# Performance work log

Hardware: AMD Instinct MI355X
Metric: run time of the kernel (lower is better)

Reference implementation:

```python
import jax, jax.numpy as jnp
import numpy as np

ALPHA = 0.2          # LeakyReLU negative slope
NEG_BIG = -9e15      # mask value from original code


def setup_inputs() -> dict:
    key = jax.random.key(0)
    k1, k2, k3, k4 = jax.random.split(key, 4)
    B, N, F_in, F_out = 16, 1024, 256, 256
    x = jax.random.normal(k1, (B, N, F_in), dtype=jnp.float32)
    adj = jax.random.randint(k2, (B, N, N), 0, 2, dtype=jnp.int32)
    # xavier-uniform-like scales
    W = jax.random.normal(k3, (F_in, F_out), dtype=jnp.float32) * np.sqrt(2.0 / (F_in + F_out))
    a = jax.random.normal(k4, (2 * F_out, 1), dtype=jnp.float32) * np.sqrt(2.0 / (2 * F_out + 1))
    return {"x": x, "adj": adj, "W": W, "a": a}


def reference(x, adj, W, a):
    # x: [B,N,Fin], adj: [B,N,N] (int mask), W: [Fin,Fout], a: [2*Fout,1]
    F_out = a.shape[0] // 2
    h = jnp.einsum("bni,io->bno", x, W)            # [B,N,Fout]
    # Decompose a into left/right halves: e_ij = lrelu(a_l.h_i + a_r.h_j)
    a_l = a[:F_out, 0]                               # [Fout]
    a_r = a[F_out:, 0]                               # [Fout]
    el = h @ a_l                                     # [B,N] score contribution of target i
    er = h @ a_r                                     # [B,N] score contribution of source j
    e = jax.nn.leaky_relu(el[:, :, None] + er[:, None, :], ALPHA)  # [B,N,N]
    e = jnp.where(adj > 0, e, NEG_BIG)
    attn = jax.nn.softmax(e, axis=-1)                # masked softmax over neighbors j
    # weighted sum of neighbor features; concat with n_heads=1 is identity
    return jnp.einsum("bij,bjo->bio", attn, h)       # [B,N,Fout]
```

## Files before the change

kernel.cpp:

```cpp
#include <hip/hip_runtime.h>
#include <stdint.h>

#define ALPHA 0.2f
#define NEG_BIG -9000000000000000.0f

typedef __attribute__((ext_vector_type(8))) short bf16x8;
typedef __attribute__((ext_vector_type(8))) unsigned short u16x8;
typedef __attribute__((ext_vector_type(4))) float f32x4;

__device__ __forceinline__ unsigned short f2bf(float f) {
    unsigned int u = __float_as_uint(f);
    u += 0x7fffu + ((u >> 16) & 1u);
    return (unsigned short)(u >> 16);
}

__device__ __forceinline__ void gload_lds16(const void* g, void* l) {
    __builtin_amdgcn_global_load_lds(
        (const __attribute__((address_space(1))) unsigned int*)g,
        (__attribute__((address_space(3))) unsigned int*)l, 16, 0, 0);
}

__global__ void wt_wa_kernel(const float* __restrict__ W,
                             const float* __restrict__ a,
                             unsigned short* __restrict__ Wtbf,
                             float* __restrict__ wa) {
    const int t = threadIdx.x;
    if (blockIdx.x < 256) {
        const int o = blockIdx.x;
        Wtbf[o * 256 + t] = f2bf(W[t * 256 + o]);
    } else {
        float sl = 0.f, sr = 0.f;
        const float* wr = W + t * 256;
        for (int o = 0; o < 256; ++o) {
            const float wv = wr[o];
            sl += wv * a[o];
            sr += wv * a[256 + o];
        }
        wa[t] = sl;
        wa[256 + t] = sr;
    }
}

__global__ __launch_bounds__(256) void eler2x_kernel(
    const float* __restrict__ x, const float* __restrict__ wa,
    float* __restrict__ el, float* __restrict__ er,
    unsigned short* __restrict__ xbf)
{
    const int w = threadIdx.x >> 6, l = threadIdx.x & 63;
    const int r = blockIdx.x * 4 + w;
    const float4 xv = *(const float4*)(x + (size_t)r * 256 + l * 4);
    const float4 al = *(const float4*)(wa + l * 4);
    const float4 ar = *(const float4*)(wa + 256 + l * 4);

    ushort4 xb;
    xb.x = f2bf(xv.x); xb.y = f2bf(xv.y); xb.z = f2bf(xv.z); xb.w = f2bf(xv.w);
    *(ushort4*)(xbf + (size_t)r * 256 + l * 4) = xb;

    float sl = xv.x * al.x + xv.y * al.y + xv.z * al.z + xv.w * al.w;
    float sr = xv.x * ar.x + xv.y * ar.y + xv.z * ar.z + xv.w * ar.w;
#pragma unroll
    for (int off = 32; off >= 1; off >>= 1) {
        sl += __shfl_xor(sl, off);
        sr += __shfl_xor(sr, off);
    }
    if (l == 0) { el[r] = sl; er[r] = sr; }
}

__global__ __launch_bounds__(256) void gemm_h(
    const unsigned short* __restrict__ A,
    const unsigned short* __restrict__ Bt,
    unsigned short* __restrict__ C)
{
    __shared__ __align__(16) unsigned short As[64 * 64];
    __shared__ __align__(16) unsigned short Bs[128 * 64];

    const int tid = threadIdx.x;
    const int w = tid >> 6, l = tid & 63;
    const int q = l >> 4, ml = l & 15;
    const int wm = (w >> 1) * 32;
    const int wn = (w & 1) * 64;
    const int m0 = blockIdx.y * 64;
    const int n0 = blockIdx.x * 128;

    f32x4 acc[2][4];
    for (int i = 0; i < 2; ++i)
        for (int j = 0; j < 4; ++j) {
            f32x4 z = {0.f, 0.f, 0.f, 0.f};
            acc[i][j] = z;
        }

    for (int k0 = 0; k0 < 256; k0 += 64) {
        for (int c = 0; c < 2; ++c) {
            const int cb = c * 256 + (w << 6);
            const int p = cb + l;
            const int r = p >> 3;
            const int cc = (p & 7) ^ (r & 7);
            gload_lds16(A + (size_t)(m0 + r) * 256 + k0 + cc * 8, As + cb * 8);
        }
        for (int c = 0; c < 4; ++c) {
            const int cb = c * 256 + (w << 6);
            const int p = cb + l;
            const int r = p >> 3;
            const int cc = (p & 7) ^ (r & 7);
            gload_lds16(Bt + (size_t)(n0 + r) * 256 + k0 + cc * 8, Bs + cb * 8);
        }
        __syncthreads();

        bf16x8 aF[2][2], bF[2][4];
#pragma unroll
        for (int ks = 0; ks < 2; ++ks) {
#pragma unroll
            for (int mt = 0; mt < 2; ++mt) {
                const int mm = wm + mt * 16 + ml;
                aF[ks][mt] = *(const bf16x8*)(As + (mm * 8 + ((ks * 4 + q) ^ (mm & 7))) * 8);
            }
#pragma unroll
            for (int nt = 0; nt < 4; ++nt) {
                const int nn = wn + nt * 16 + ml;
                bF[ks][nt] = *(const bf16x8*)(Bs + (nn * 8 + ((ks * 4 + q) ^ (nn & 7))) * 8);
            }
        }
#pragma unroll
        for (int ks = 0; ks < 2; ++ks)
            for (int mt = 0; mt < 2; ++mt)
                for (int nt = 0; nt < 4; ++nt)
                    acc[mt][nt] = __builtin_amdgcn_mfma_f32_16x16x32_bf16(
                        aF[ks][mt], bF[ks][nt], acc[mt][nt], 0, 0, 0);
        __syncthreads();
    }

    for (int mt = 0; mt < 2; ++mt)
        for (int nt = 0; nt < 4; ++nt) {
            const int gn = n0 + wn + nt * 16 + ml;
            for (int r = 0; r < 4; ++r) {
                const int gm = m0 + wm + mt * 16 + q * 4 + r;
                C[(size_t)gm * 16384 + gn] = f2bf(acc[mt][nt][r]);
            }
        }
}

__global__ __launch_bounds__(256) void mask_kernel(
    const int* __restrict__ adj,
    const float* __restrict__ el,
    const float* __restrict__ er,
    float* __restrict__ c,
    unsigned short* __restrict__ pk16)
{
    __shared__ unsigned char nibs[4][256];

    const int w = threadIdx.x >> 6, l = threadIdx.x & 63;
    const int row = blockIdx.x * 4 + w;
    const int b = row >> 10;
    const int* arow = adj + (size_t)row * 1024;
    const float* erb = er + (b << 10);
    const float eli = el[row];

    float ev[16];
    float m = -3.0e38f;
#pragma unroll
    for (int it = 0; it < 4; ++it) {
        const int j = it * 256 + l * 4;
        const int4 av = *(const int4*)(arow + j);
        const float4 erv = *(const float4*)(erb + j);
        float e0 = eli + erv.x; e0 = e0 > 0.f ? e0 : ALPHA * e0; e0 = av.x > 0 ? e0 : NEG_BIG;
        float e1 = eli + erv.y; e1 = e1 > 0.f ? e1 : ALPHA * e1; e1 = av.y > 0 ? e1 : NEG_BIG;
        float e2 = eli + erv.z; e2 = e2 > 0.f ? e2 : ALPHA * e2; e2 = av.z > 0 ? e2 : NEG_BIG;
        float e3 = eli + erv.w; e3 = e3 > 0.f ? e3 : ALPHA * e3; e3 = av.w > 0 ? e3 : NEG_BIG;
        ev[it * 4 + 0] = e0; ev[it * 4 + 1] = e1;
        ev[it * 4 + 2] = e2; ev[it * 4 + 3] = e3;
        m = fmaxf(m, fmaxf(fmaxf(e0, e1), fmaxf(e2, e3)));
        nibs[w][it * 64 + l] =
            (unsigned char)((av.x > 0) | ((av.y > 0) << 1) |
                            ((av.z > 0) << 2) | ((av.w > 0) << 3));
    }
#pragma unroll
    for (int off = 32; off >= 1; off >>= 1) m = fmaxf(m, __shfl_xor(m, off));
    float s = 0.f;
#pragma unroll
    for (int u = 0; u < 16; ++u) s += __expf(ev[u] - m);
#pragma unroll
    for (int off = 32; off >= 1; off >>= 1) s += __shfl_xor(s, off);
    if (l == 0) c[row] = m + __logf(s);

    const unsigned nr = *(const unsigned int*)(&nibs[w][l * 4]);
    const unsigned short mask16 =
        (unsigned short)((nr & 0xFu) | ((nr >> 4) & 0xF0u) |
                         ((nr >> 8) & 0xF00u) | ((nr >> 12) & 0xF000u));
    pk16[(size_t)row * 64 + l] = mask16;
}

__global__ __launch_bounds__(256) void pv_kernel(
    const unsigned short* __restrict__ pk16,
    const float* __restrict__ el,
    const float* __restrict__ er,
    const float* __restrict__ c,
    const unsigned short* __restrict__ hT,
    float* __restrict__ out)
{
    __shared__ float er_s[1024];
    __shared__ __align__(16) unsigned short pk_s[32 * 64];
    __shared__ __align__(16) unsigned short Hs[256 * 64];
    __shared__ __align__(16) unsigned short Ps[32 * 72];

    const int tid = threadIdx.x;
    const int w = tid >> 6, l = tid & 63;
    const int q = l >> 4, ml = l & 15;
    const int b = blockIdx.y;
    const int i0 = blockIdx.x * 32;

    *(float4*)(er_s + tid * 4) = *(const float4*)(er + (b << 10) + tid * 4);
    *(u16x8*)(pk_s + tid * 8) =
        *(const u16x8*)(pk16 + ((size_t)(b << 10) + i0) * 64 + tid * 8);
    const int ib = tid >> 3;
    const int js = (tid & 7) * 8;
    const float eli_b = el[(b << 10) + i0 + ib];
    const float ci = c[(b << 10) + i0 + ib];
    __syncthreads();

    f32x4 acc[2][4];
    for (int i = 0; i < 2; ++i)
        for (int j = 0; j < 4; ++j) {
            f32x4 z = {0.f, 0.f, 0.f, 0.f};
            acc[i][j] = z;
        }

    const unsigned short* hb = hT + (size_t)b * 1024;

    for (int j0 = 0; j0 < 1024; j0 += 64) {
        for (int cr = 0; cr < 8; ++cr) {
            const int cb = cr * 256 + (w << 6);
            const int p = cb + l;
            const int r = p >> 3;
            const int cc = (p & 7) ^ (r & 7);
            gload_lds16(hb + (size_t)r * 16384 + j0 + cc * 8, Hs + cb * 8);
        }
        {
            const unsigned hw = pk_s[ib * 64 + ((j0 + js) >> 4)];
            const unsigned v = (hw >> ((j0 + js) & 15)) & 0xFFu;
            u16x8 pvv;
#pragma unroll
            for (int u = 0; u < 8; ++u) {
                float e = eli_b + er_s[j0 + js + u];
                e = e > 0.f ? e : ALPHA * e;
                const float p = ((v >> u) & 1u) ? __expf(e - ci) : 0.f;
                pvv[u] = f2bf(p);
            }
            *(u16x8*)(Ps + ib * 72 + js) = pvv;
        }
        __syncthreads();

        bf16x8 aF[2][2], bF[2][4];
#pragma unroll
        for (int ks = 0; ks < 2; ++ks) {
#pragma unroll
            for (int mt = 0; mt < 2; ++mt)
                aF[ks][mt] = *(const bf16x8*)(Ps + (mt * 16 + ml) * 72 + ks * 32 + q * 8);
#pragma unroll
            for (int nt = 0; nt < 4; ++nt) {
                const int oc = (w << 6) + nt * 16 + ml;
                bF[ks][nt] = *(const bf16x8*)(Hs + (oc * 8 + ((ks * 4 + q) ^ (oc & 7))) * 8);
            }
        }
#pragma unroll
        for (int ks = 0; ks < 2; ++ks)
            for (int mt = 0; mt < 2; ++mt)
                for (int nt = 0; nt < 4; ++nt)
                    acc[mt][nt] = __builtin_amdgcn_mfma_f32_16x16x32_bf16(
                        aF[ks][mt], bF[ks][nt], acc[mt][nt], 0, 0, 0);
        __syncthreads();
    }

    float* ob = out + (size_t)b * 262144;
    for (int mt = 0; mt < 2; ++mt)
        for (int nt = 0; nt < 4; ++nt) {
            const int gn = (w << 6) + nt * 16 + ml;
            for (int r = 0; r < 4; ++r) {
                const int gm = i0 + mt * 16 + q * 4 + r;
                ob[(size_t)gm * 256 + gn] = acc[mt][nt][r];
            }
        }
}

extern "C" void kernel_launch(void* const* d_in, const int* in_sizes, int n_in,
                              void* d_out, int out_size, void* d_ws, size_t ws_size,
                              hipStream_t stream) {
    const float* x   = (const float*)d_in[0];
    const int*   adj = (const int*)d_in[1];
    const float* W   = (const float*)d_in[2];
    const float* a   = (const float*)d_in[3];
    float* out = (float*)d_out;

    char* ws = (char*)d_ws;
    unsigned short* Wtbf  = (unsigned short*)(ws);
    float* wa             = (float*)(ws + 131072);
    unsigned short* xbf   = (unsigned short*)(ws + 133120);
    unsigned short* h_T   = (unsigned short*)(ws + 8521728);
    float* el             = (float*)(ws + 16910336);
    float* er             = (float*)(ws + 16975872);
    float* c              = (float*)(ws + 17041408);
    unsigned short* pk16  = (unsigned short*)(ws + 17106944);

    wt_wa_kernel<<<dim3(257), dim3(256), 0, stream>>>(W, a, Wtbf, wa);

    eler2x_kernel<<<dim3(4096), dim3(256), 0, stream>>>(x, wa, el, er, xbf);

    gemm_h<<<dim3(128, 4), dim3(256), 0, stream>>>(Wtbf, xbf, h_T);

    mask_kernel<<<dim3(4096), dim3(256), 0, stream>>>(adj, el, er, c, pk16);

    pv_kernel<<<dim3(32, 16), dim3(256), 0, stream>>>(pk16, el, er, c, h_T, out);
}
```

Before: 156.3 us.

## Restructure PV kernel with direct-register H loads, double-buffered P tiles, exp2 scaling

The PV kernel now uses 512-thread blocks over 64 rows, with blocks mapped so batches are interleaved. It loads H fragments straight from global memory into registers, one tile ahead, instead of staging them through LDS. P tiles are double-buffered in LDS and guarded by a lighter barrier that waits only on LDS counters, so building the next P tile overlaps the MFMA work. Scores are prescaled by log2(e) so the kernels can call exp2/log2 directly, and the launch grid shrinks from 512 blocks to 256. The risks are uncoalesced H reads from global memory and reduced parallelism, since each block now covers more rows.

```diff
diff --git a/kernel.cpp b/kernel.cpp
--- a/kernel.cpp
+++ b/kernel.cpp
@@ -3,6 +3,7 @@
 
 #define ALPHA 0.2f
 #define NEG_BIG -9000000000000000.0f
+#define L2E 1.4426950408889634f
 
 typedef __attribute__((ext_vector_type(8))) short bf16x8;
 typedef __attribute__((ext_vector_type(8))) unsigned short u16x8;
@@ -18,6 +19,11 @@
     __builtin_amdgcn_global_load_lds(
         (const __attribute__((address_space(1))) unsigned int*)g,
         (__attribute__((address_space(3))) unsigned int*)l, 16, 0, 0);
+}
+
+__device__ __forceinline__ void bar_lds() {
+    asm volatile("s_waitcnt lgkmcnt(0)" ::: "memory");
+    __builtin_amdgcn_s_barrier();
 }
 
 __global__ void wt_wa_kernel(const float* __restrict__ W,
@@ -63,7 +69,7 @@
         sl += __shfl_xor(sl, off);
         sr += __shfl_xor(sr, off);
     }
-    if (l == 0) { el[r] = sl; er[r] = sr; }
+    if (l == 0) { el[r] = sl * L2E; er[r] = sr * L2E; }
 }
 
 __global__ __launch_bounds__(256) void gemm_h(
@@ -177,10 +183,10 @@
     for (int off = 32; off >= 1; off >>= 1) m = fmaxf(m, __shfl_xor(m, off));
     float s = 0.f;
 #pragma unroll
-    for (int u = 0; u < 16; ++u) s += __expf(ev[u] - m);
+    for (int u = 0; u < 16; ++u) s += exp2f(ev[u] - m);
 #pragma unroll
     for (int off = 32; off >= 1; off >>= 1) s += __shfl_xor(s, off);
-    if (l == 0) c[row] = m + __logf(s);
+    if (l == 0) c[row] = m + log2f(s);
 
     const unsigned nr = *(const unsigned int*)(&nibs[w][l * 4]);
     const unsigned short mask16 =
@@ -189,93 +195,129 @@
     pk16[(size_t)row * 64 + l] = mask16;
 }
 
-__global__ __launch_bounds__(256) void pv_kernel(
+__global__ __launch_bounds__(512, 2) void pv_kernel(
     const unsigned short* __restrict__ pk16,
-    const float* __restrict__ el,
-    const float* __restrict__ er,
-    const float* __restrict__ c,
+    const float* __restrict__ el2,
+    const float* __restrict__ er2,
+    const float* __restrict__ c2,
     const unsigned short* __restrict__ hT,
     float* __restrict__ out)
 {
     __shared__ float er_s[1024];
-    __shared__ __align__(16) unsigned short pk_s[32 * 64];
-    __shared__ __align__(16) unsigned short Hs[256 * 64];
-    __shared__ __align__(16) unsigned short Ps[32 * 72];
+    __shared__ __align__(16) unsigned short pk_s[64 * 72];
+    __shared__ __align__(16) unsigned short Ps[2 * 64 * 72];
 
     const int tid = threadIdx.x;
     const int w = tid >> 6, l = tid & 63;
     const int q = l >> 4, ml = l & 15;
-    const int b = blockIdx.y;
-    const int i0 = blockIdx.x * 32;
-
-    *(float4*)(er_s + tid * 4) = *(const float4*)(er + (b << 10) + tid * 4);
-    *(u16x8*)(pk_s + tid * 8) =
-        *(const u16x8*)(pk16 + ((size_t)(b << 10) + i0) * 64 + tid * 8);
+    const int wm = (w >> 2) * 32;
+    const int wn = (w & 3) * 64;
+
+    const int lin = blockIdx.x;
+    const int b = ((lin & 7) << 1) | ((lin >> 3) & 1);
+    const int i0 = (lin >> 4) * 64;
+
+    *(float2*)(er_s + tid * 2) = *(const float2*)(er2 + (b << 10) + tid * 2);
+    {
+        const int pr = tid >> 3, pc = (tid & 7) * 8;
+        *(u16x8*)(pk_s + pr * 72 + pc) =
+            *(const u16x8*)(pk16 + ((size_t)((b << 10) + i0 + pr)) * 64 + pc);
+    }
+
     const int ib = tid >> 3;
     const int js = (tid & 7) * 8;
-    const float eli_b = el[(b << 10) + i0 + ib];
-    const float ci = c[(b << 10) + i0 + ib];
-    __syncthreads();
+    const int rg = (b << 10) + i0 + ib;
+    const float el2i = el2[rg];
+    const float c2i = c2[rg];
 
     f32x4 acc[2][4];
+#pragma unroll
     for (int i = 0; i < 2; ++i)
+#pragma unroll
         for (int j = 0; j < 4; ++j) {
             f32x4 z = {0.f, 0.f, 0.f, 0.f};
             acc[i][j] = z;
         }
 
     const unsigned short* hb = hT + (size_t)b * 1024;
-
-    for (int j0 = 0; j0 < 1024; j0 += 64) {
-        for (int cr = 0; cr < 8; ++cr) {
-            const int cb = cr * 256 + (w << 6);
-            const int p = cb + l;
-            const int r = p >> 3;
-            const int cc = (p & 7) ^ (r & 7);
-            gload_lds16(hb + (size_t)r * 16384 + j0 + cc * 8, Hs + cb * 8);
-        }
-        {
-            const unsigned hw = pk_s[ib * 64 + ((j0 + js) >> 4)];
-            const unsigned v = (hw >> ((j0 + js) & 15)) & 0xFFu;
-            u16x8 pvv;
-#pragma unroll
-            for (int u = 0; u < 8; ++u) {
-                float e = eli_b + er_s[j0 + js + u];
-                e = e > 0.f ? e : ALPHA * e;
-                const float p = ((v >> u) & 1u) ? __expf(e - ci) : 0.f;
-                pvv[u] = f2bf(p);
-            }
-            *(u16x8*)(Ps + ib * 72 + js) = pvv;
-        }
-        __syncthreads();
-
-        bf16x8 aF[2][2], bF[2][4];
-#pragma unroll
-        for (int ks = 0; ks < 2; ++ks) {
-#pragma unroll
-            for (int mt = 0; mt < 2; ++mt)
-                aF[ks][mt] = *(const bf16x8*)(Ps + (mt * 16 + ml) * 72 + ks * 32 + q * 8);
-#pragma unroll
-            for (int nt = 0; nt < 4; ++nt) {
-                const int oc = (w << 6) + nt * 16 + ml;
-                bF[ks][nt] = *(const bf16x8*)(Hs + (oc * 8 + ((ks * 4 + q) ^ (oc & 7))) * 8);
-            }
-        }
-#pragma unroll
-        for (int ks = 0; ks < 2; ++ks)
-            for (int mt = 0; mt < 2; ++mt)
-                for (int nt = 0; nt < 4; ++nt)
-                    acc[mt][nt] = __builtin_amdgcn_mfma_f32_16x16x32_bf16(
-                        aF[ks][mt], bF[ks][nt], acc[mt][nt], 0, 0, 0);
-        __syncthreads();
-    }
+    const unsigned short* bp[4];
+#pragma unroll
+    for (int nt = 0; nt < 4; ++nt)
+        bp[nt] = hb + (size_t)(wn + nt * 16 + ml) * 16384 + q * 8;
+
+    bf16x8 B0[2][4], B1[2][4];
+
+#define LOADB(B, t) do {                                                      \
+    _Pragma("unroll")                                                         \
+    for (int nt_ = 0; nt_ < 4; ++nt_) {                                       \
+        B[0][nt_] = *(const bf16x8*)(bp[nt_] + (t) * 64);                     \
+        B[1][nt_] = *(const bf16x8*)(bp[nt_] + (t) * 64 + 32);                \
+    } } while (0)
+
+#define BUILD(BI, t) do {                                                     \
+    const int j0_ = (t) * 64;                                                 \
+    float ev8[8];                                                             \
+    *(f32x4*)(ev8)     = *(const f32x4*)(er_s + j0_ + js);                    \
+    *(f32x4*)(ev8 + 4) = *(const f32x4*)(er_s + j0_ + js + 4);                \
+    const unsigned hw_ = pk_s[ib * 72 + ((j0_ + js) >> 4)];                   \
+    const unsigned mv_ = (hw_ >> (js & 8)) & 0xFFu;                           \
+    u16x8 pv_;                                                                \
+    _Pragma("unroll")                                                         \
+    for (int u_ = 0; u_ < 8; ++u_) {                                          \
+        float e_ = el2i + ev8[u_];                                            \
+        e_ = fmaxf(e_, ALPHA * e_);         \
+        float p_ = exp2f(e_ - c2i);                                           \
+        p_ = ((mv_ >> u_) & 1u) ? p_ : 0.f;                                   \
+        pv_[u_] = f2bf(p_);                                                   \
+    }                                                                         \
+    *(u16x8*)(Ps + (BI) * (64 * 72) + ib * 72 + js) = pv_;                    \
+    } while (0)
+
+#define COMPUTE(BI, B) do {                                                   \
+    bf16x8 aF[2][2];                                                          \
+    _Pragma("unroll")                                                         \
+    for (int ks_ = 0; ks_ < 2; ++ks_)                                         \
+        _Pragma("unroll")                                                     \
+        for (int mt_ = 0; mt_ < 2; ++mt_)                                     \
+            aF[ks_][mt_] = *(const bf16x8*)(Ps + (BI) * (64 * 72) +           \
+                (wm + mt_ * 16 + ml) * 72 + ks_ * 32 + q * 8);                \
+    _Pragma("unroll")                                                         \
+    for (int ks_ = 0; ks_ < 2; ++ks_)                                         \
+        _Pragma("unroll")                                                     \
+        for (int mt_ = 0; mt_ < 2; ++mt_)                                     \
+            _Pragma("unroll")                                                 \
+            for (int nt_ = 0; nt_ < 4; ++nt_)                                 \
+                acc[mt_][nt_] = __builtin_amdgcn_mfma_f32_16x16x32_bf16(      \
+                    aF[ks_][mt_], B[ks_][nt_], acc[mt_][nt_], 0, 0, 0);       \
+    } while (0)
+
+    __syncthreads();
+    LOADB(B0, 0);
+
+    for (int t = 0; t < 16; t += 2) {
+        BUILD(0, t);
+        LOADB(B1, t + 1);
+        bar_lds();
+        COMPUTE(0, B0);
+        BUILD(1, t + 1);
+        if (t + 2 < 16) LOADB(B0, t + 2);
+        bar_lds();
+        COMPUTE(1, B1);
+    }
+
+#undef LOADB
+#undef BUILD
+#undef COMPUTE
 
     float* ob = out + (size_t)b * 262144;
+#pragma unroll
     for (int mt = 0; mt < 2; ++mt)
+#pragma unroll
         for (int nt = 0; nt < 4; ++nt) {
-            const int gn = (w << 6) + nt * 16 + ml;
+            const int gn = wn + nt * 16 + ml;
+#pragma unroll
             for (int r = 0; r < 4; ++r) {
-                const int gm = i0 + mt * 16 + q * 4 + r;
+                const int gm = i0 + wm + mt * 16 + q * 4 + r;
                 ob[(size_t)gm * 256 + gn] = acc[mt][nt][r];
             }
         }
@@ -308,5 +350,5 @@
 
     mask_kernel<<<dim3(4096), dim3(256), 0, stream>>>(adj, el, er, c, pk16);
 
-    pv_kernel<<<dim3(32, 16), dim3(256), 0, stream>>>(pk16, el, er, c, h_T, out);
-}
+    pv_kernel<<<dim3(256), dim3(512), 0, stream>>>(pk16, el, er, c, h_T, out);
+}
```

New measurement: 164.3 us. 1.05x slower.
